# Kernel tuning notes

Measured on AMD Instinct MI355X. Metric: run time of the kernel, lower is better.

The kernel has to match this reference:

```python
import jax, jax.numpy as jnp
import numpy as np

B, N, F = 2, 512, 128
NUM_BASIS = 4


def _mlp(x, W1, b1, W2, b2, W3, b3):
    # two hidden ReLU layers, linear output -> [..., NUM_BASIS]
    h = jax.nn.relu(x @ W1 + b1)
    h = jax.nn.relu(h @ W2 + b2)
    return h @ W3 + b3


def setup_inputs() -> dict:
    key = jax.random.key(0)
    ks = jax.random.split(key, 12)
    s = 0.05  # keep activations O(1)
    inp = {
        "pointwise_features": jax.random.normal(ks[0], (B, N, F), jnp.float32),
        "relative_features": jax.random.normal(ks[1], (B, N, N, F), jnp.float32),
        "pointwise_basis": jax.random.normal(ks[2], (B, N, NUM_BASIS, 3), jnp.float32),
        "relative_basis": jax.random.normal(ks[3], (B, N, N, NUM_BASIS, 3), jnp.float32),
        "pw_W1": jax.random.normal(ks[4], (F, 128), jnp.float32) * s,
        "pw_b1": jnp.zeros((128,), jnp.float32),
        "pw_W2": jax.random.normal(ks[5], (128, 128), jnp.float32) * s,
        "pw_b2": jnp.zeros((128,), jnp.float32),
        "pw_W3": jax.random.normal(ks[6], (128, NUM_BASIS), jnp.float32) * s,
        "pw_b3": jnp.zeros((NUM_BASIS,), jnp.float32),
        "rel_W1": jax.random.normal(ks[7], (F, 128), jnp.float32) * s,
        "rel_b1": jnp.zeros((128,), jnp.float32),
        "rel_W2": jax.random.normal(ks[8], (128, 128), jnp.float32) * s,
        "rel_b2": jnp.zeros((128,), jnp.float32),
        "rel_W3": jax.random.normal(ks[9], (128, NUM_BASIS), jnp.float32) * s,
        "rel_b3": jnp.zeros((NUM_BASIS,), jnp.float32),
        # last 64 atoms are padding (masked) in every batch element
        "masked_elements": jnp.broadcast_to(jnp.arange(N) >= N - 64, (B, N)),
    }
    return inp


def reference(pointwise_features, relative_features, pointwise_basis, relative_basis,
              pw_W1, pw_b1, pw_W2, pw_b2, pw_W3, pw_b3,
              rel_W1, rel_b1, rel_W2, rel_b2, rel_W3, rel_b3,
              masked_elements):
    unmasked = ~masked_elements                      # [B, N]
    num_atoms = unmasked.sum(-1).astype(pointwise_features.dtype)  # [B]

    # pointwise_shift: [B, N, K, 3]
    pw_scale = _mlp(pointwise_features, pw_W1, pw_b1, pw_W2, pw_b2, pw_W3, pw_b3)
    pointwise_shift = pointwise_basis * pw_scale[..., None]

    # relative_shift: [B, N, N, K, 3], mask over j, mean over j
    rel_scale = _mlp(relative_features, rel_W1, rel_b1, rel_W2, rel_b2, rel_W3, rel_b3)
    relative_shift = relative_basis * rel_scale[..., None]
    relative_shift = relative_shift * unmasked[:, None, :, None, None]
    relative_shift = relative_shift.sum(-3) / num_atoms[:, None, None, None]  # [B, N, K, 3]

    all_shifts = pointwise_shift + relative_shift
    shift = all_shifts.sum(-2) / num_atoms[:, None, None]  # [B, N, 3]
    return shift
```

## Files before the change

kernel.cpp:

```cpp
#include <hip/hip_runtime.h>
#include <stdint.h>

#define LDK 136

typedef __attribute__((ext_vector_type(4))) float f32x4;
typedef __attribute__((ext_vector_type(8))) short bf16x8;

__device__ inline unsigned short f2bf_rtne(float f) {
    union { float f; unsigned u; } v; v.f = f;
    unsigned u = v.u;
    u += 0x7fffu + ((u >> 16) & 1u);
    return (unsigned short)(u >> 16);
}

__global__ void prep_kernel(const float* __restrict__ relW1, const float* __restrict__ relW2,
                            const float* __restrict__ pwW1, const float* __restrict__ pwW2,
                            const float* __restrict__ relW3, const float* __restrict__ pwW3,
                            const void* __restrict__ maskp,
                            float* __restrict__ maskf, float* __restrict__ na,
                            int* __restrict__ gflag, float* __restrict__ out,
                            unsigned short* __restrict__ w1T_rel, unsigned short* __restrict__ w2T_rel,
                            unsigned short* __restrict__ w1T_pw, unsigned short* __restrict__ w2T_pw,
                            unsigned short* __restrict__ w3T_rel, unsigned short* __restrict__ w3T_pw) {
    int t = threadIdx.x;
    const float* srcs[4] = {relW1, relW2, pwW1, pwW2};
    unsigned short* dsts[4] = {w1T_rel, w2T_rel, w1T_pw, w2T_pw};
    int e0 = blockIdx.x * 1024 + t;
#pragma unroll
    for (int i = 0; i < 4; ++i) {
        int e = e0 + i * 256;
        int mat = e >> 14, o = e & 16383;
        int n = o >> 7, k = o & 127;
        dsts[mat][o] = f2bf_rtne(srcs[mat][k * 128 + n]);
    }
    if (blockIdx.x == 1) {
        for (int i = t; i < 2048; i += 256) {
            int r = i >> 7, h = i & 127;
            w3T_rel[i] = (r < 4) ? f2bf_rtne(relW3[h * 4 + r]) : (unsigned short)0;
            w3T_pw[i]  = (r < 4) ? f2bf_rtne(pwW3[h * 4 + r])  : (unsigned short)0;
        }
    }
    if (blockIdx.x == 2) {
        for (int i = t; i < 3072; i += 256) out[i] = 0.f;
    }
    if (blockIdx.x == 0) {
        __shared__ int anyb;
        __shared__ float cnt[2];
        if (t == 0) anyb = 0;
        if (t < 2) cnt[t] = 0.f;
        __syncthreads();
        const unsigned char* mb = (const unsigned char*)maskp;
        int la = 0;
        for (int i = t; i < 1024; i += 256) la |= mb[i];
        if (la) atomicOr(&anyb, 1);
        __syncthreads();
        bool isbyte = (anyb != 0);
        const int* mi = (const int*)maskp;
        float loc0 = 0.f, loc1 = 0.f;
        for (int i = t; i < 1024; i += 256) {
            int v = isbyte ? (int)mb[i] : mi[i];
            float um = (v != 0) ? 0.f : 1.f;
            maskf[i] = um;
            if (i < 512) loc0 += um; else loc1 += um;
        }
        atomicAdd(&cnt[0], loc0);
        atomicAdd(&cnt[1], loc1);
        __syncthreads();
        if (t < 2) na[t] = cnt[t];
        if (t < 16) {
            float s = 0.f;
            for (int j = 0; j < 64; ++j) s += maskf[t * 64 + j];
            gflag[t] = (s > 0.f) ? 1 : 0;
        }
    }
}

__global__ __launch_bounds__(256, 3)
void mlp_kernel(const float* __restrict__ Xrel, const float* __restrict__ Xpw,
                const unsigned short* __restrict__ w1Tr, const unsigned short* __restrict__ w2Tr,
                const unsigned short* __restrict__ w3Tr,
                const unsigned short* __restrict__ w1Tp, const unsigned short* __restrict__ w2Tp,
                const unsigned short* __restrict__ w3Tp,
                const float* __restrict__ b1r, const float* __restrict__ b2r, const float* __restrict__ b3r,
                const float* __restrict__ b1p, const float* __restrict__ b2p, const float* __restrict__ b3p,
                const float* __restrict__ rel_basis, const float* __restrict__ pw_basis,
                const float* __restrict__ maskf, const float* __restrict__ na,
                const int* __restrict__ gflag,
                float* __restrict__ out) {
    __shared__ short xs[64 * LDK];
    __shared__ short hs[64 * LDK];
    __shared__ short w3s[16 * LDK];
    __shared__ float bs1[128], bs2[128], b3s[4];
    __shared__ float Sl[256];
    __shared__ float red[4][3];

    int t = threadIdx.x;
    int w = t >> 6, lane = t & 63, q = lane >> 4, col = lane & 15;

    bool isrel = (blockIdx.x >= 4);
    int rb = isrel ? ((int)blockIdx.x - 4) : (int)blockIdx.x;

    const float* X = isrel ? Xrel : Xpw;
    const unsigned short* w1T = isrel ? w1Tr : w1Tp;
    const unsigned short* w2T = isrel ? w2Tr : w2Tp;
    const unsigned short* w3T = isrel ? w3Tr : w3Tp;
    const float* b1 = isrel ? b1r : b1p;
    const float* b2 = isrel ? b2r : b2p;
    const float* b3 = isrel ? b3r : b3p;

    if (t < 128) { bs1[t] = b1[t]; bs2[t] = b2[t]; }
    if (t < 4) b3s[t] = b3[t];
    for (int i = t; i < 2048; i += 256) {
        int r = i >> 7, c = i & 127;
        w3s[r * LDK + c] = w3T[i];
    }

    int b = isrel ? (rb >> 10) : (rb >> 1);
    float NA = na[b];
    float scale = isrel ? (1.f / (NA * NA)) : (1.f / NA);

    int apack = 0x3210, nact = 4;
    if (isrel) {
        apack = 0; nact = 0;
        int gbase = b * 8 + (rb & 1) * 4;
#pragma unroll
        for (int tt = 0; tt < 4; ++tt)
            if (gflag[gbase + tt]) { apack |= tt << (4 * nact); ++nact; }
        if (nact == 0) return;
    }

    bf16x8 w1f[2][4], w2f[2][4];
#pragma unroll
    for (int tn = 0; tn < 2; ++tn)
#pragma unroll
        for (int kc = 0; kc < 4; ++kc) {
            int n = w * 32 + tn * 16 + col;
            int kk = kc * 32 + q * 8;
            w1f[tn][kc] = *(const bf16x8*)&w1T[n * 128 + kk];
            w2f[tn][kc] = *(const bf16x8*)&w2T[n * 128 + kk];
        }

    long rowbase = (long)rb * 256;
    int r0 = t >> 5, cg = t & 31;
    int myrow = w * 16 + col;
    int arow = t >> 2, ak = t & 3;

    float4 px[8];
    {
        const float4* Xg = (const float4*)(X + (rowbase + (long)(apack & 15) * 64) * 128);
#pragma unroll
        for (int i = 0; i < 8; ++i) px[i] = Xg[(r0 + 8 * i) * 32 + cg];
#pragma unroll
        for (int i = 0; i < 8; ++i) {
            float4 v = px[i];
            short4 s4 = make_short4((short)f2bf_rtne(v.x), (short)f2bf_rtne(v.y),
                                    (short)f2bf_rtne(v.z), (short)f2bf_rtne(v.w));
            *(short4*)&xs[(r0 + 8 * i) * LDK + cg * 4] = s4;
        }
    }
    __syncthreads();

    float p0 = 0.f, p1 = 0.f, p2 = 0.f;

    for (int a = 0; a < nact; ++a) {
        int tile = (apack >> (4 * a)) & 15;
        long trow = rowbase + (long)tile * 64;

        if (a + 1 < nact) {
            int tnx = (apack >> (4 * (a + 1))) & 15;
            const float4* Xg2 = (const float4*)(X + (rowbase + (long)tnx * 64) * 128);
#pragma unroll
            for (int i = 0; i < 8; ++i) px[i] = Xg2[(r0 + 8 * i) * 32 + cg];
        }

        f32x4 acc[2][4];
#pragma unroll
        for (int tn = 0; tn < 2; ++tn)
#pragma unroll
            for (int tm = 0; tm < 4; ++tm) acc[tn][tm] = (f32x4)(0.f);
#pragma unroll
        for (int kc = 0; kc < 4; ++kc) {
            bf16x8 bf[4];
#pragma unroll
            for (int tm = 0; tm < 4; ++tm)
                bf[tm] = *(const bf16x8*)&xs[(tm * 16 + col) * LDK + kc * 32 + q * 8];
#pragma unroll
            for (int tn = 0; tn < 2; ++tn)
#pragma unroll
                for (int tm = 0; tm < 4; ++tm)
                    acc[tn][tm] = __builtin_amdgcn_mfma_f32_16x16x32_bf16(w1f[tn][kc], bf[tm], acc[tn][tm], 0, 0, 0);
        }

#pragma unroll
        for (int tn = 0; tn < 2; ++tn)
#pragma unroll
            for (int tm = 0; tm < 4; ++tm) {
                int n0 = w * 32 + tn * 16 + q * 4;
                int m = tm * 16 + col;
                float4 bb = *(const float4*)&bs1[n0];
                short4 s4 = make_short4(
                    (short)f2bf_rtne(fmaxf(acc[tn][tm][0] + bb.x, 0.f)),
                    (short)f2bf_rtne(fmaxf(acc[tn][tm][1] + bb.y, 0.f)),
                    (short)f2bf_rtne(fmaxf(acc[tn][tm][2] + bb.z, 0.f)),
                    (short)f2bf_rtne(fmaxf(acc[tn][tm][3] + bb.w, 0.f)));
                *(short4*)&hs[m * LDK + n0] = s4;
            }
        __syncthreads();

        if (a + 1 < nact) {
#pragma unroll
            for (int i = 0; i < 8; ++i) {
                float4 v = px[i];
                short4 s4 = make_short4((short)f2bf_rtne(v.x), (short)f2bf_rtne(v.y),
                                        (short)f2bf_rtne(v.z), (short)f2bf_rtne(v.w));
                *(short4*)&xs[(r0 + 8 * i) * LDK + cg * 4] = s4;
            }
        }

        float bas0 = 0.f, bas1 = 0.f, bas2 = 0.f, mrow = 1.f;
        if (isrel) {
            const float* bp = &rel_basis[(trow + arow) * 12 + ak * 3];
            bas0 = bp[0]; bas1 = bp[1]; bas2 = bp[2];
            mrow = maskf[b * 512 + (rb & 1) * 256 + tile * 64 + myrow];
        }

        f32x4 acc2[2][4];
#pragma unroll
        for (int tn = 0; tn < 2; ++tn)
#pragma unroll
            for (int tm = 0; tm < 4; ++tm) acc2[tn][tm] = (f32x4)(0.f);
#pragma unroll
        for (int kc = 0; kc < 4; ++kc) {
            bf16x8 bf[4];
#pragma unroll
            for (int tm = 0; tm < 4; ++tm)
                bf[tm] = *(const bf16x8*)&hs[(tm * 16 + col) * LDK + kc * 32 + q * 8];
#pragma unroll
            for (int tn = 0; tn < 2; ++tn)
#pragma unroll
                for (int tm = 0; tm < 4; ++tm)
                    acc2[tn][tm] = __builtin_amdgcn_mfma_f32_16x16x32_bf16(w2f[tn][kc], bf[tm], acc2[tn][tm], 0, 0, 0);
        }
        __syncthreads();

#pragma unroll
        for (int tn = 0; tn < 2; ++tn)
#pragma unroll
            for (int tm = 0; tm < 4; ++tm) {
                int n0 = w * 32 + tn * 16 + q * 4;
                int m = tm * 16 + col;
                float4 bb = *(const float4*)&bs2[n0];
                short4 s4 = make_short4(
                    (short)f2bf_rtne(fmaxf(acc2[tn][tm][0] + bb.x, 0.f)),
                    (short)f2bf_rtne(fmaxf(acc2[tn][tm][1] + bb.y, 0.f)),
                    (short)f2bf_rtne(fmaxf(acc2[tn][tm][2] + bb.z, 0.f)),
                    (short)f2bf_rtne(fmaxf(acc2[tn][tm][3] + bb.w, 0.f)));
                *(short4*)&hs[m * LDK + n0] = s4;
            }
        __syncthreads();

        {
            f32x4 a3 = (f32x4)(0.f);
#pragma unroll
            for (int kc = 0; kc < 4; ++kc) {
                bf16x8 w3fk = *(const bf16x8*)&w3s[col * LDK + kc * 32 + q * 8];
                bf16x8 hb = *(const bf16x8*)&hs[(w * 16 + col) * LDK + kc * 32 + q * 8];
                a3 = __builtin_amdgcn_mfma_f32_16x16x32_bf16(w3fk, hb, a3, 0, 0, 0);
            }
            if (isrel) {
                if (q == 0) {
                    float4 sm = make_float4((a3[0] + b3s[0]) * mrow, (a3[1] + b3s[1]) * mrow,
                                            (a3[2] + b3s[2]) * mrow, (a3[3] + b3s[3]) * mrow);
                    *(float4*)&Sl[myrow * 4] = sm;
                }
            } else if (q == 0) {
                long bi = trow + myrow;
                float s0 = a3[0] + b3s[0], s1 = a3[1] + b3s[1];
                float s2 = a3[2] + b3s[2], s3 = a3[3] + b3s[3];
                const float* pbp = &pw_basis[bi * 12];
                float o0 = s0 * pbp[0] + s1 * pbp[3] + s2 * pbp[6] + s3 * pbp[9];
                float o1 = s0 * pbp[1] + s1 * pbp[4] + s2 * pbp[7] + s3 * pbp[10];
                float o2 = s0 * pbp[2] + s1 * pbp[5] + s2 * pbp[8] + s3 * pbp[11];
                atomicAdd(&out[bi * 3 + 0], o0 * scale);
                atomicAdd(&out[bi * 3 + 1], o1 * scale);
                atomicAdd(&out[bi * 3 + 2], o2 * scale);
            }
        }
        __syncthreads();

        if (isrel) {
            float sk = Sl[arow * 4 + ak];
            p0 += sk * bas0; p1 += sk * bas1; p2 += sk * bas2;
        }
    }

    if (isrel) {
#pragma unroll
        for (int s = 32; s >= 4; s >>= 1) {
            p0 += __shfl_down(p0, s);
            p1 += __shfl_down(p1, s);
            p2 += __shfl_down(p2, s);
        }
        p0 += __shfl_down(p0, 2); p1 += __shfl_down(p1, 2); p2 += __shfl_down(p2, 2);
        p0 += __shfl_down(p0, 1); p1 += __shfl_down(p1, 1); p2 += __shfl_down(p2, 1);
        if (lane == 0) { red[w][0] = p0; red[w][1] = p1; red[w][2] = p2; }
        __syncthreads();
        if (t < 3) {
            float v = red[0][t] + red[1][t] + red[2][t] + red[3][t];
            atomicAdd(&out[(long)(rb >> 1) * 3 + t], v * scale);
        }
    }
}

extern "C" void kernel_launch(void* const* d_in, const int* in_sizes, int n_in,
                              void* d_out, int out_size, void* d_ws, size_t ws_size,
                              hipStream_t stream) {
    const float* pw_feat   = (const float*)d_in[0];
    const float* rel_feat  = (const float*)d_in[1];
    const float* pw_basis  = (const float*)d_in[2];
    const float* rel_basis = (const float*)d_in[3];
    const float* pw_W1 = (const float*)d_in[4];
    const float* pw_b1 = (const float*)d_in[5];
    const float* pw_W2 = (const float*)d_in[6];
    const float* pw_b2 = (const float*)d_in[7];
    const float* pw_W3 = (const float*)d_in[8];
    const float* pw_b3 = (const float*)d_in[9];
    const float* rel_W1 = (const float*)d_in[10];
    const float* rel_b1 = (const float*)d_in[11];
    const float* rel_W2 = (const float*)d_in[12];
    const float* rel_b2 = (const float*)d_in[13];
    const float* rel_W3 = (const float*)d_in[14];
    const float* rel_b3 = (const float*)d_in[15];
    const void*  maskp  = d_in[16];
    float* out = (float*)d_out;

    char* ws = (char*)d_ws;
    float* maskf = (float*)(ws + 0);
    float* na    = (float*)(ws + 4096);
    int*   gflag = (int*)(ws + 4160);
    unsigned short* w1T_rel = (unsigned short*)(ws + 4352);
    unsigned short* w2T_rel = (unsigned short*)(ws + 37120);
    unsigned short* w1T_pw  = (unsigned short*)(ws + 69888);
    unsigned short* w2T_pw  = (unsigned short*)(ws + 102656);
    unsigned short* w3T_rel = (unsigned short*)(ws + 135424);
    unsigned short* w3T_pw  = (unsigned short*)(ws + 139520);

    prep_kernel<<<64, 256, 0, stream>>>(rel_W1, rel_W2, pw_W1, pw_W2, rel_W3, pw_W3, maskp,
                                        maskf, na, gflag, out,
                                        w1T_rel, w2T_rel, w1T_pw, w2T_pw,
                                        w3T_rel, w3T_pw);
    mlp_kernel<<<2052, 256, 0, stream>>>(rel_feat, pw_feat,
                                         w1T_rel, w2T_rel, w3T_rel,
                                         w1T_pw, w2T_pw, w3T_pw,
                                         rel_b1, rel_b2, rel_b3,
                                         pw_b1, pw_b2, pw_b3,
                                         rel_basis, pw_basis, maskf, na, gflag, out);
}
```

Before: 524.6 us.

## Process two row tiles per iteration with double-buffered LDS staging

Restructures the per-block tile loop so two 64-row tiles are handled per iteration, using separate A/B buffers for both the input and hidden activations. This cuts barriers per tile and lets the layer-2 and layer-3 work of one tile overlap the epilogue and staging of the other. Layer-3 weights now live in registers instead of LDS. The doubled shared-memory footprint and higher register pressure lower occupancy, which is reflected in dropping launch bounds from 3 to 2 blocks per CU.

```diff
diff --git a/kernel.cpp b/kernel.cpp
--- a/kernel.cpp
+++ b/kernel.cpp
@@ -75,7 +75,96 @@
     }
 }
 
-__global__ __launch_bounds__(256, 3)
+__device__ __forceinline__ void zero_acc(f32x4 (&acc)[2][4]) {
+#pragma unroll
+    for (int tn = 0; tn < 2; ++tn)
+#pragma unroll
+        for (int tm = 0; tm < 4; ++tm) acc[tn][tm] = (f32x4)(0.f);
+}
+
+__device__ __forceinline__ void mfma_layer(const short* src, const bf16x8 (&wf)[2][4],
+                                           f32x4 (&acc)[2][4], int col, int q) {
+#pragma unroll
+    for (int kc = 0; kc < 4; ++kc) {
+        bf16x8 bf[4];
+#pragma unroll
+        for (int tm = 0; tm < 4; ++tm)
+            bf[tm] = *(const bf16x8*)&src[(tm * 16 + col) * LDK + kc * 32 + q * 8];
+#pragma unroll
+        for (int tn = 0; tn < 2; ++tn)
+#pragma unroll
+            for (int tm = 0; tm < 4; ++tm)
+                acc[tn][tm] = __builtin_amdgcn_mfma_f32_16x16x32_bf16(wf[tn][kc], bf[tm], acc[tn][tm], 0, 0, 0);
+    }
+}
+
+__device__ __forceinline__ void epi_relu_store(const f32x4 (&acc)[2][4], const float* bs,
+                                               short* dst, int w, int q, int col) {
+#pragma unroll
+    for (int tn = 0; tn < 2; ++tn)
+#pragma unroll
+        for (int tm = 0; tm < 4; ++tm) {
+            int n0 = w * 32 + tn * 16 + q * 4;
+            int m = tm * 16 + col;
+            float4 bb = *(const float4*)&bs[n0];
+            short4 s4 = make_short4(
+                (short)f2bf_rtne(fmaxf(acc[tn][tm][0] + bb.x, 0.f)),
+                (short)f2bf_rtne(fmaxf(acc[tn][tm][1] + bb.y, 0.f)),
+                (short)f2bf_rtne(fmaxf(acc[tn][tm][2] + bb.z, 0.f)),
+                (short)f2bf_rtne(fmaxf(acc[tn][tm][3] + bb.w, 0.f)));
+            *(short4*)&dst[m * LDK + n0] = s4;
+        }
+}
+
+__device__ __forceinline__ void load_px(const float* X, long trow, float4 (&v)[8], int r0, int cg) {
+    const float4* Xg = (const float4*)(X + trow * 128);
+#pragma unroll
+    for (int i = 0; i < 8; ++i) v[i] = Xg[(r0 + 8 * i) * 32 + cg];
+}
+
+__device__ __forceinline__ void stage_conv(const float4 (&v)[8], short* dst, int r0, int cg) {
+#pragma unroll
+    for (int i = 0; i < 8; ++i) {
+        float4 vv = v[i];
+        short4 s4 = make_short4((short)f2bf_rtne(vv.x), (short)f2bf_rtne(vv.y),
+                                (short)f2bf_rtne(vv.z), (short)f2bf_rtne(vv.w));
+        *(short4*)&dst[(r0 + 8 * i) * LDK + cg * 4] = s4;
+    }
+}
+
+__device__ __forceinline__ f32x4 layer3(const short* hsrc, const bf16x8 (&w3f)[4],
+                                        int w, int col, int q) {
+    f32x4 a3 = (f32x4)(0.f);
+#pragma unroll
+    for (int kc = 0; kc < 4; ++kc) {
+        bf16x8 hb = *(const bf16x8*)&hsrc[(w * 16 + col) * LDK + kc * 32 + q * 8];
+        a3 = __builtin_amdgcn_mfma_f32_16x16x32_bf16(w3f[kc], hb, a3, 0, 0, 0);
+    }
+    return a3;
+}
+
+__device__ __forceinline__ void l3_epi(f32x4 a3, bool isrel, int q, int myrow,
+                                       const float* b3s, float mrow, float* Slx,
+                                       long trow, const float* __restrict__ pw_basis,
+                                       float scale, float* __restrict__ out) {
+    if (q != 0) return;
+    float s0 = a3[0] + b3s[0], s1 = a3[1] + b3s[1];
+    float s2 = a3[2] + b3s[2], s3 = a3[3] + b3s[3];
+    if (isrel) {
+        *(float4*)&Slx[myrow * 4] = make_float4(s0 * mrow, s1 * mrow, s2 * mrow, s3 * mrow);
+    } else {
+        long bi = trow + myrow;
+        const float* pbp = &pw_basis[bi * 12];
+        float o0 = s0 * pbp[0] + s1 * pbp[3] + s2 * pbp[6] + s3 * pbp[9];
+        float o1 = s0 * pbp[1] + s1 * pbp[4] + s2 * pbp[7] + s3 * pbp[10];
+        float o2 = s0 * pbp[2] + s1 * pbp[5] + s2 * pbp[8] + s3 * pbp[11];
+        atomicAdd(&out[bi * 3 + 0], o0 * scale);
+        atomicAdd(&out[bi * 3 + 1], o1 * scale);
+        atomicAdd(&out[bi * 3 + 2], o2 * scale);
+    }
+}
+
+__global__ __launch_bounds__(256, 2)
 void mlp_kernel(const float* __restrict__ Xrel, const float* __restrict__ Xpw,
                 const unsigned short* __restrict__ w1Tr, const unsigned short* __restrict__ w2Tr,
                 const unsigned short* __restrict__ w3Tr,
@@ -87,11 +176,10 @@
                 const float* __restrict__ maskf, const float* __restrict__ na,
                 const int* __restrict__ gflag,
                 float* __restrict__ out) {
-    __shared__ short xs[64 * LDK];
-    __shared__ short hs[64 * LDK];
-    __shared__ short w3s[16 * LDK];
+    __shared__ short xsA[64 * LDK], xsB[64 * LDK];
+    __shared__ short hsA[64 * LDK], hsB[64 * LDK];
     __shared__ float bs1[128], bs2[128], b3s[4];
-    __shared__ float Sl[256];
+    __shared__ float Sl[2][256];
     __shared__ float red[4][3];
 
     int t = threadIdx.x;
@@ -110,10 +198,6 @@
 
     if (t < 128) { bs1[t] = b1[t]; bs2[t] = b2[t]; }
     if (t < 4) b3s[t] = b3[t];
-    for (int i = t; i < 2048; i += 256) {
-        int r = i >> 7, c = i & 127;
-        w3s[r * LDK + c] = w3T[i];
-    }
 
     int b = isrel ? (rb >> 10) : (rb >> 1);
     float NA = na[b];
@@ -129,7 +213,7 @@
         if (nact == 0) return;
     }
 
-    bf16x8 w1f[2][4], w2f[2][4];
+    bf16x8 w1f[2][4], w2f[2][4], w3f[4];
 #pragma unroll
     for (int tn = 0; tn < 2; ++tn)
 #pragma unroll
@@ -139,170 +223,126 @@
             w1f[tn][kc] = *(const bf16x8*)&w1T[n * 128 + kk];
             w2f[tn][kc] = *(const bf16x8*)&w2T[n * 128 + kk];
         }
+#pragma unroll
+    for (int kc = 0; kc < 4; ++kc)
+        w3f[kc] = *(const bf16x8*)&w3T[col * 128 + kc * 32 + q * 8];
 
     long rowbase = (long)rb * 256;
     int r0 = t >> 5, cg = t & 31;
     int myrow = w * 16 + col;
     int arow = t >> 2, ak = t & 3;
+    int mbase = b * 512 + (rb & 1) * 256;
 
     float4 px[8];
-    {
-        const float4* Xg = (const float4*)(X + (rowbase + (long)(apack & 15) * 64) * 128);
-#pragma unroll
-        for (int i = 0; i < 8; ++i) px[i] = Xg[(r0 + 8 * i) * 32 + cg];
-#pragma unroll
-        for (int i = 0; i < 8; ++i) {
-            float4 v = px[i];
-            short4 s4 = make_short4((short)f2bf_rtne(v.x), (short)f2bf_rtne(v.y),
-                                    (short)f2bf_rtne(v.z), (short)f2bf_rtne(v.w));
-            *(short4*)&xs[(r0 + 8 * i) * LDK + cg * 4] = s4;
-        }
+    load_px(X, rowbase + (long)(apack & 15) * 64, px, r0, cg);
+    stage_conv(px, xsA, r0, cg);
+    if (nact >= 2) {
+        load_px(X, rowbase + (long)((apack >> 4) & 15) * 64, px, r0, cg);
+        stage_conv(px, xsB, r0, cg);
     }
     __syncthreads();
 
     float p0 = 0.f, p1 = 0.f, p2 = 0.f;
-
-    for (int a = 0; a < nact; ++a) {
-        int tile = (apack >> (4 * a)) & 15;
-        long trow = rowbase + (long)tile * 64;
-
-        if (a + 1 < nact) {
-            int tnx = (apack >> (4 * (a + 1))) & 15;
-            const float4* Xg2 = (const float4*)(X + (rowbase + (long)tnx * 64) * 128);
-#pragma unroll
-            for (int i = 0; i < 8; ++i) px[i] = Xg2[(r0 + 8 * i) * 32 + cg];
-        }
-
-        f32x4 acc[2][4];
-#pragma unroll
-        for (int tn = 0; tn < 2; ++tn)
-#pragma unroll
-            for (int tm = 0; tm < 4; ++tm) acc[tn][tm] = (f32x4)(0.f);
-#pragma unroll
-        for (int kc = 0; kc < 4; ++kc) {
-            bf16x8 bf[4];
-#pragma unroll
-            for (int tm = 0; tm < 4; ++tm)
-                bf[tm] = *(const bf16x8*)&xs[(tm * 16 + col) * LDK + kc * 32 + q * 8];
-#pragma unroll
-            for (int tn = 0; tn < 2; ++tn)
-#pragma unroll
-                for (int tm = 0; tm < 4; ++tm)
-                    acc[tn][tm] = __builtin_amdgcn_mfma_f32_16x16x32_bf16(w1f[tn][kc], bf[tm], acc[tn][tm], 0, 0, 0);
-        }
-
-#pragma unroll
-        for (int tn = 0; tn < 2; ++tn)
-#pragma unroll
-            for (int tm = 0; tm < 4; ++tm) {
-                int n0 = w * 32 + tn * 16 + q * 4;
-                int m = tm * 16 + col;
-                float4 bb = *(const float4*)&bs1[n0];
-                short4 s4 = make_short4(
-                    (short)f2bf_rtne(fmaxf(acc[tn][tm][0] + bb.x, 0.f)),
-                    (short)f2bf_rtne(fmaxf(acc[tn][tm][1] + bb.y, 0.f)),
-                    (short)f2bf_rtne(fmaxf(acc[tn][tm][2] + bb.z, 0.f)),
-                    (short)f2bf_rtne(fmaxf(acc[tn][tm][3] + bb.w, 0.f)));
-                *(short4*)&hs[m * LDK + n0] = s4;
-            }
-        __syncthreads();
-
-        if (a + 1 < nact) {
-#pragma unroll
-            for (int i = 0; i < 8; ++i) {
-                float4 v = px[i];
-                short4 s4 = make_short4((short)f2bf_rtne(v.x), (short)f2bf_rtne(v.y),
-                                        (short)f2bf_rtne(v.z), (short)f2bf_rtne(v.w));
-                *(short4*)&xs[(r0 + 8 * i) * LDK + cg * 4] = s4;
-            }
-        }
-
-        float bas0 = 0.f, bas1 = 0.f, bas2 = 0.f, mrow = 1.f;
-        if (isrel) {
-            const float* bp = &rel_basis[(trow + arow) * 12 + ak * 3];
-            bas0 = bp[0]; bas1 = bp[1]; bas2 = bp[2];
-            mrow = maskf[b * 512 + (rb & 1) * 256 + tile * 64 + myrow];
-        }
-
-        f32x4 acc2[2][4];
-#pragma unroll
-        for (int tn = 0; tn < 2; ++tn)
-#pragma unroll
-            for (int tm = 0; tm < 4; ++tm) acc2[tn][tm] = (f32x4)(0.f);
-#pragma unroll
-        for (int kc = 0; kc < 4; ++kc) {
-            bf16x8 bf[4];
-#pragma unroll
-            for (int tm = 0; tm < 4; ++tm)
-                bf[tm] = *(const bf16x8*)&hs[(tm * 16 + col) * LDK + kc * 32 + q * 8];
-#pragma unroll
-            for (int tn = 0; tn < 2; ++tn)
-#pragma unroll
-                for (int tm = 0; tm < 4; ++tm)
-                    acc2[tn][tm] = __builtin_amdgcn_mfma_f32_16x16x32_bf16(w2f[tn][kc], bf[tm], acc2[tn][tm], 0, 0, 0);
-        }
-        __syncthreads();
-
-#pragma unroll
-        for (int tn = 0; tn < 2; ++tn)
-#pragma unroll
-            for (int tm = 0; tm < 4; ++tm) {
-                int n0 = w * 32 + tn * 16 + q * 4;
-                int m = tm * 16 + col;
-                float4 bb = *(const float4*)&bs2[n0];
-                short4 s4 = make_short4(
-                    (short)f2bf_rtne(fmaxf(acc2[tn][tm][0] + bb.x, 0.f)),
-                    (short)f2bf_rtne(fmaxf(acc2[tn][tm][1] + bb.y, 0.f)),
-                    (short)f2bf_rtne(fmaxf(acc2[tn][tm][2] + bb.z, 0.f)),
-                    (short)f2bf_rtne(fmaxf(acc2[tn][tm][3] + bb.w, 0.f)));
-                *(short4*)&hs[m * LDK + n0] = s4;
-            }
-        __syncthreads();
-
+    f32x4 acc[2][4];
+
+    int a = 0;
+    for (; a + 1 < nact; a += 2) {
+        int tA = (apack >> (4 * a)) & 15;
+        int tB = (apack >> (4 * (a + 1))) & 15;
+        long trA = rowbase + (long)tA * 64;
+        long trB = rowbase + (long)tB * 64;
+        bool hN0 = (a + 2 < nact);
+        bool hN1 = (a + 3 < nact);
+
+        if (hN0) load_px(X, rowbase + (long)((apack >> (4 * (a + 2))) & 15) * 64, px, r0, cg);
+        zero_acc(acc);
+        mfma_layer(xsA, w1f, acc, col, q);
+        epi_relu_store(acc, bs1, hsA, w, q, col);
+        zero_acc(acc);
+        mfma_layer(xsB, w1f, acc, col, q);
+        epi_relu_store(acc, bs1, hsB, w, q, col);
+        __syncthreads();
+
+        if (hN0) stage_conv(px, xsA, r0, cg);
+        if (hN1) load_px(X, rowbase + (long)((apack >> (4 * (a + 3))) & 15) * 64, px, r0, cg);
+        float baA0 = 0.f, baA1 = 0.f, baA2 = 0.f, baB0 = 0.f, baB1 = 0.f, baB2 = 0.f;
+        float mrA = 1.f, mrB = 1.f;
+        if (isrel) {
+            const float* bpA = &rel_basis[(trA + arow) * 12 + ak * 3];
+            baA0 = bpA[0]; baA1 = bpA[1]; baA2 = bpA[2];
+            const float* bpB = &rel_basis[(trB + arow) * 12 + ak * 3];
+            baB0 = bpB[0]; baB1 = bpB[1]; baB2 = bpB[2];
+            mrA = maskf[mbase + tA * 64 + myrow];
+            mrB = maskf[mbase + tB * 64 + myrow];
+        }
+        zero_acc(acc);
+        mfma_layer(hsA, w2f, acc, col, q);
+        __syncthreads();
+
+        epi_relu_store(acc, bs2, hsA, w, q, col);
+        zero_acc(acc);
+        mfma_layer(hsB, w2f, acc, col, q);
+        __syncthreads();
+
+        epi_relu_store(acc, bs2, hsB, w, q, col);
         {
-            f32x4 a3 = (f32x4)(0.f);
-#pragma unroll
-            for (int kc = 0; kc < 4; ++kc) {
-                bf16x8 w3fk = *(const bf16x8*)&w3s[col * LDK + kc * 32 + q * 8];
-                bf16x8 hb = *(const bf16x8*)&hs[(w * 16 + col) * LDK + kc * 32 + q * 8];
-                a3 = __builtin_amdgcn_mfma_f32_16x16x32_bf16(w3fk, hb, a3, 0, 0, 0);
-            }
-            if (isrel) {
-                if (q == 0) {
-                    float4 sm = make_float4((a3[0] + b3s[0]) * mrow, (a3[1] + b3s[1]) * mrow,
-                                            (a3[2] + b3s[2]) * mrow, (a3[3] + b3s[3]) * mrow);
-                    *(float4*)&Sl[myrow * 4] = sm;
-                }
-            } else if (q == 0) {
-                long bi = trow + myrow;
-                float s0 = a3[0] + b3s[0], s1 = a3[1] + b3s[1];
-                float s2 = a3[2] + b3s[2], s3 = a3[3] + b3s[3];
-                const float* pbp = &pw_basis[bi * 12];
-                float o0 = s0 * pbp[0] + s1 * pbp[3] + s2 * pbp[6] + s3 * pbp[9];
-                float o1 = s0 * pbp[1] + s1 * pbp[4] + s2 * pbp[7] + s3 * pbp[10];
-                float o2 = s0 * pbp[2] + s1 * pbp[5] + s2 * pbp[8] + s3 * pbp[11];
-                atomicAdd(&out[bi * 3 + 0], o0 * scale);
-                atomicAdd(&out[bi * 3 + 1], o1 * scale);
-                atomicAdd(&out[bi * 3 + 2], o2 * scale);
-            }
-        }
-        __syncthreads();
-
-        if (isrel) {
-            float sk = Sl[arow * 4 + ak];
-            p0 += sk * bas0; p1 += sk * bas1; p2 += sk * bas2;
+            f32x4 a3 = layer3(hsA, w3f, w, col, q);
+            l3_epi(a3, isrel, q, myrow, b3s, mrA, Sl[0], trA, pw_basis, scale, out);
+        }
+        if (hN1) stage_conv(px, xsB, r0, cg);
+        __syncthreads();
+
+        {
+            f32x4 a3 = layer3(hsB, w3f, w, col, q);
+            l3_epi(a3, isrel, q, myrow, b3s, mrB, Sl[1], trB, pw_basis, scale, out);
+        }
+        if (isrel) {
+            float sk = Sl[0][arow * 4 + ak];
+            p0 += sk * baA0; p1 += sk * baA1; p2 += sk * baA2;
+        }
+        __syncthreads();
+        if (isrel) {
+            float sk = Sl[1][arow * 4 + ak];
+            p0 += sk * baB0; p1 += sk * baB1; p2 += sk * baB2;
+        }
+    }
+
+    if (a < nact) {
+        int tA = (apack >> (4 * a)) & 15;
+        long trA = rowbase + (long)tA * 64;
+        float baA0 = 0.f, baA1 = 0.f, baA2 = 0.f, mrA = 1.f;
+        if (isrel) {
+            const float* bpA = &rel_basis[(trA + arow) * 12 + ak * 3];
+            baA0 = bpA[0]; baA1 = bpA[1]; baA2 = bpA[2];
+            mrA = maskf[mbase + tA * 64 + myrow];
+        }
+        zero_acc(acc);
+        mfma_layer(xsA, w1f, acc, col, q);
+        epi_relu_store(acc, bs1, hsA, w, q, col);
+        __syncthreads();
+        zero_acc(acc);
+        mfma_layer(hsA, w2f, acc, col, q);
+        __syncthreads();
+        epi_relu_store(acc, bs2, hsA, w, q, col);
+        __syncthreads();
+        {
+            f32x4 a3 = layer3(hsA, w3f, w, col, q);
+            l3_epi(a3, isrel, q, myrow, b3s, mrA, Sl[0], trA, pw_basis, scale, out);
+        }
+        __syncthreads();
+        if (isrel) {
+            float sk = Sl[0][arow * 4 + ak];
+            p0 += sk * baA0; p1 += sk * baA1; p2 += sk * baA2;
         }
     }
 
     if (isrel) {
 #pragma unroll
-        for (int s = 32; s >= 4; s >>= 1) {
+        for (int s = 32; s > 0; s >>= 1) {
             p0 += __shfl_down(p0, s);
             p1 += __shfl_down(p1, s);
             p2 += __shfl_down(p2, s);
         }
-        p0 += __shfl_down(p0, 2); p1 += __shfl_down(p1, 2); p2 += __shfl_down(p2, 2);
-        p0 += __shfl_down(p0, 1); p1 += __shfl_down(p1, 1); p2 += __shfl_down(p2, 1);
         if (lane == 0) { red[w][0] = p0; red[w][1] = p1; red[w][2] = p2; }
         __syncthreads();
         if (t < 3) {
```

Measured after the change: 446.5 us. 14.9% less time.

## Use 512-thread blocks with 8 waves each owning 16 hidden columns

Applied to the files above, without the earlier changes.

Doubles the MLP kernel's block size to 8 waves, so each wave computes one 16-wide output column tile instead of two. This halves per-thread weight fragments, accumulators and prefetch registers to allow more waves in flight. It also moves the rel_basis and mask loads ahead of the first GEMM so their latency overlaps compute. The layer-3 and reduction stages still use only 4 waves, so half the threads sit idle there, and the extra synchronisation cost across more waves may offset the gain.

```diff
diff --git a/kernel.cpp b/kernel.cpp
--- a/kernel.cpp
+++ b/kernel.cpp
@@ -75,7 +75,7 @@
     }
 }
 
-__global__ __launch_bounds__(256, 3)
+__global__ __launch_bounds__(512, 4)
 void mlp_kernel(const float* __restrict__ Xrel, const float* __restrict__ Xpw,
                 const unsigned short* __restrict__ w1Tr, const unsigned short* __restrict__ w2Tr,
                 const unsigned short* __restrict__ w3Tr,
@@ -95,7 +95,7 @@
     __shared__ float red[4][3];
 
     int t = threadIdx.x;
-    int w = t >> 6, lane = t & 63, q = lane >> 4, col = lane & 15;
+    int wv = t >> 6, lane = t & 63, q = lane >> 4, col = lane & 15;
 
     bool isrel = (blockIdx.x >= 4);
     int rb = isrel ? ((int)blockIdx.x - 4) : (int)blockIdx.x;
@@ -110,9 +110,8 @@
 
     if (t < 128) { bs1[t] = b1[t]; bs2[t] = b2[t]; }
     if (t < 4) b3s[t] = b3[t];
-    for (int i = t; i < 2048; i += 256) {
-        int r = i >> 7, c = i & 127;
-        w3s[r * LDK + c] = w3T[i];
+    for (int i = t; i < 2048; i += 512) {
+        w3s[(i >> 7) * LDK + (i & 127)] = w3T[i];
     }
 
     int b = isrel ? (rb >> 10) : (rb >> 1);
@@ -129,33 +128,32 @@
         if (nact == 0) return;
     }
 
-    bf16x8 w1f[2][4], w2f[2][4];
-#pragma unroll
-    for (int tn = 0; tn < 2; ++tn)
-#pragma unroll
-        for (int kc = 0; kc < 4; ++kc) {
-            int n = w * 32 + tn * 16 + col;
-            int kk = kc * 32 + q * 8;
-            w1f[tn][kc] = *(const bf16x8*)&w1T[n * 128 + kk];
-            w2f[tn][kc] = *(const bf16x8*)&w2T[n * 128 + kk];
-        }
+    bf16x8 w1f[4], w2f[4];
+#pragma unroll
+    for (int kc = 0; kc < 4; ++kc) {
+        int n = wv * 16 + col;
+        int kk = kc * 32 + q * 8;
+        w1f[kc] = *(const bf16x8*)&w1T[n * 128 + kk];
+        w2f[kc] = *(const bf16x8*)&w2T[n * 128 + kk];
+    }
 
     long rowbase = (long)rb * 256;
     int r0 = t >> 5, cg = t & 31;
-    int myrow = w * 16 + col;
+    int myrow = wv * 16 + col;
     int arow = t >> 2, ak = t & 3;
-
-    float4 px[8];
+    int mbase = b * 512 + (rb & 1) * 256;
+
+    float4 px[4];
     {
         const float4* Xg = (const float4*)(X + (rowbase + (long)(apack & 15) * 64) * 128);
 #pragma unroll
-        for (int i = 0; i < 8; ++i) px[i] = Xg[(r0 + 8 * i) * 32 + cg];
-#pragma unroll
-        for (int i = 0; i < 8; ++i) {
+        for (int i = 0; i < 4; ++i) px[i] = Xg[(r0 + 16 * i) * 32 + cg];
+#pragma unroll
+        for (int i = 0; i < 4; ++i) {
             float4 v = px[i];
             short4 s4 = make_short4((short)f2bf_rtne(v.x), (short)f2bf_rtne(v.y),
                                     (short)f2bf_rtne(v.z), (short)f2bf_rtne(v.w));
-            *(short4*)&xs[(r0 + 8 * i) * LDK + cg * 4] = s4;
+            *(short4*)&xs[(r0 + 16 * i) * LDK + cg * 4] = s4;
         }
     }
     __syncthreads();
@@ -170,14 +168,21 @@
             int tnx = (apack >> (4 * (a + 1))) & 15;
             const float4* Xg2 = (const float4*)(X + (rowbase + (long)tnx * 64) * 128);
 #pragma unroll
-            for (int i = 0; i < 8; ++i) px[i] = Xg2[(r0 + 8 * i) * 32 + cg];
-        }
-
-        f32x4 acc[2][4];
-#pragma unroll
-        for (int tn = 0; tn < 2; ++tn)
-#pragma unroll
-            for (int tm = 0; tm < 4; ++tm) acc[tn][tm] = (f32x4)(0.f);
+            for (int i = 0; i < 4; ++i) px[i] = Xg2[(r0 + 16 * i) * 32 + cg];
+        }
+
+        float bas0 = 0.f, bas1 = 0.f, bas2 = 0.f, mrow = 1.f;
+        if (isrel) {
+            if (t < 256) {
+                const float* bp = &rel_basis[(trow + arow) * 12 + ak * 3];
+                bas0 = bp[0]; bas1 = bp[1]; bas2 = bp[2];
+            }
+            if (wv < 4 && q == 0) mrow = maskf[mbase + tile * 64 + myrow];
+        }
+
+        f32x4 acc[4];
+#pragma unroll
+        for (int tm = 0; tm < 4; ++tm) acc[tm] = (f32x4)(0.f);
 #pragma unroll
         for (int kc = 0; kc < 4; ++kc) {
             bf16x8 bf[4];
@@ -185,50 +190,37 @@
             for (int tm = 0; tm < 4; ++tm)
                 bf[tm] = *(const bf16x8*)&xs[(tm * 16 + col) * LDK + kc * 32 + q * 8];
 #pragma unroll
-            for (int tn = 0; tn < 2; ++tn)
-#pragma unroll
-                for (int tm = 0; tm < 4; ++tm)
-                    acc[tn][tm] = __builtin_amdgcn_mfma_f32_16x16x32_bf16(w1f[tn][kc], bf[tm], acc[tn][tm], 0, 0, 0);
-        }
-
-#pragma unroll
-        for (int tn = 0; tn < 2; ++tn)
-#pragma unroll
-            for (int tm = 0; tm < 4; ++tm) {
-                int n0 = w * 32 + tn * 16 + q * 4;
-                int m = tm * 16 + col;
-                float4 bb = *(const float4*)&bs1[n0];
-                short4 s4 = make_short4(
-                    (short)f2bf_rtne(fmaxf(acc[tn][tm][0] + bb.x, 0.f)),
-                    (short)f2bf_rtne(fmaxf(acc[tn][tm][1] + bb.y, 0.f)),
-                    (short)f2bf_rtne(fmaxf(acc[tn][tm][2] + bb.z, 0.f)),
-                    (short)f2bf_rtne(fmaxf(acc[tn][tm][3] + bb.w, 0.f)));
-                *(short4*)&hs[m * LDK + n0] = s4;
-            }
+            for (int tm = 0; tm < 4; ++tm)
+                acc[tm] = __builtin_amdgcn_mfma_f32_16x16x32_bf16(w1f[kc], bf[tm], acc[tm], 0, 0, 0);
+        }
+
+#pragma unroll
+        for (int tm = 0; tm < 4; ++tm) {
+            int n0 = wv * 16 + q * 4;
+            int m = tm * 16 + col;
+            float4 bb = *(const float4*)&bs1[n0];
+            short4 s4 = make_short4(
+                (short)f2bf_rtne(fmaxf(acc[tm][0] + bb.x, 0.f)),
+                (short)f2bf_rtne(fmaxf(acc[tm][1] + bb.y, 0.f)),
+                (short)f2bf_rtne(fmaxf(acc[tm][2] + bb.z, 0.f)),
+                (short)f2bf_rtne(fmaxf(acc[tm][3] + bb.w, 0.f)));
+            *(short4*)&hs[m * LDK + n0] = s4;
+        }
         __syncthreads();
 
         if (a + 1 < nact) {
 #pragma unroll
-            for (int i = 0; i < 8; ++i) {
+            for (int i = 0; i < 4; ++i) {
                 float4 v = px[i];
                 short4 s4 = make_short4((short)f2bf_rtne(v.x), (short)f2bf_rtne(v.y),
                                         (short)f2bf_rtne(v.z), (short)f2bf_rtne(v.w));
-                *(short4*)&xs[(r0 + 8 * i) * LDK + cg * 4] = s4;
+                *(short4*)&xs[(r0 + 16 * i) * LDK + cg * 4] = s4;
             }
         }
 
-        float bas0 = 0.f, bas1 = 0.f, bas2 = 0.f, mrow = 1.f;
-        if (isrel) {
-            const float* bp = &rel_basis[(trow + arow) * 12 + ak * 3];
-            bas0 = bp[0]; bas1 = bp[1]; bas2 = bp[2];
-            mrow = maskf[b * 512 + (rb & 1) * 256 + tile * 64 + myrow];
-        }
-
-        f32x4 acc2[2][4];
-#pragma unroll
-        for (int tn = 0; tn < 2; ++tn)
-#pragma unroll
-            for (int tm = 0; tm < 4; ++tm) acc2[tn][tm] = (f32x4)(0.f);
+        f32x4 acc2[4];
+#pragma unroll
+        for (int tm = 0; tm < 4; ++tm) acc2[tm] = (f32x4)(0.f);
 #pragma unroll
         for (int kc = 0; kc < 4; ++kc) {
             bf16x8 bf[4];
@@ -236,59 +228,54 @@
             for (int tm = 0; tm < 4; ++tm)
                 bf[tm] = *(const bf16x8*)&hs[(tm * 16 + col) * LDK + kc * 32 + q * 8];
 #pragma unroll
-            for (int tn = 0; tn < 2; ++tn)
-#pragma unroll
-                for (int tm = 0; tm < 4; ++tm)
-                    acc2[tn][tm] = __builtin_amdgcn_mfma_f32_16x16x32_bf16(w2f[tn][kc], bf[tm], acc2[tn][tm], 0, 0, 0);
-        }
-        __syncthreads();
-
-#pragma unroll
-        for (int tn = 0; tn < 2; ++tn)
-#pragma unroll
-            for (int tm = 0; tm < 4; ++tm) {
-                int n0 = w * 32 + tn * 16 + q * 4;
-                int m = tm * 16 + col;
-                float4 bb = *(const float4*)&bs2[n0];
-                short4 s4 = make_short4(
-                    (short)f2bf_rtne(fmaxf(acc2[tn][tm][0] + bb.x, 0.f)),
-                    (short)f2bf_rtne(fmaxf(acc2[tn][tm][1] + bb.y, 0.f)),
-                    (short)f2bf_rtne(fmaxf(acc2[tn][tm][2] + bb.z, 0.f)),
-                    (short)f2bf_rtne(fmaxf(acc2[tn][tm][3] + bb.w, 0.f)));
-                *(short4*)&hs[m * LDK + n0] = s4;
-            }
-        __syncthreads();
-
-        {
+            for (int tm = 0; tm < 4; ++tm)
+                acc2[tm] = __builtin_amdgcn_mfma_f32_16x16x32_bf16(w2f[kc], bf[tm], acc2[tm], 0, 0, 0);
+        }
+        __syncthreads();
+
+#pragma unroll
+        for (int tm = 0; tm < 4; ++tm) {
+            int n0 = wv * 16 + q * 4;
+            int m = tm * 16 + col;
+            float4 bb = *(const float4*)&bs2[n0];
+            short4 s4 = make_short4(
+                (short)f2bf_rtne(fmaxf(acc2[tm][0] + bb.x, 0.f)),
+                (short)f2bf_rtne(fmaxf(acc2[tm][1] + bb.y, 0.f)),
+                (short)f2bf_rtne(fmaxf(acc2[tm][2] + bb.z, 0.f)),
+                (short)f2bf_rtne(fmaxf(acc2[tm][3] + bb.w, 0.f)));
+            *(short4*)&hs[m * LDK + n0] = s4;
+        }
+        __syncthreads();
+
+        if (wv < 4) {
             f32x4 a3 = (f32x4)(0.f);
 #pragma unroll
             for (int kc = 0; kc < 4; ++kc) {
                 bf16x8 w3fk = *(const bf16x8*)&w3s[col * LDK + kc * 32 + q * 8];
-                bf16x8 hb = *(const bf16x8*)&hs[(w * 16 + col) * LDK + kc * 32 + q * 8];
+                bf16x8 hb = *(const bf16x8*)&hs[(wv * 16 + col) * LDK + kc * 32 + q * 8];
                 a3 = __builtin_amdgcn_mfma_f32_16x16x32_bf16(w3fk, hb, a3, 0, 0, 0);
             }
-            if (isrel) {
-                if (q == 0) {
-                    float4 sm = make_float4((a3[0] + b3s[0]) * mrow, (a3[1] + b3s[1]) * mrow,
-                                            (a3[2] + b3s[2]) * mrow, (a3[3] + b3s[3]) * mrow);
-                    *(float4*)&Sl[myrow * 4] = sm;
-                }
-            } else if (q == 0) {
-                long bi = trow + myrow;
+            if (q == 0) {
                 float s0 = a3[0] + b3s[0], s1 = a3[1] + b3s[1];
                 float s2 = a3[2] + b3s[2], s3 = a3[3] + b3s[3];
-                const float* pbp = &pw_basis[bi * 12];
-                float o0 = s0 * pbp[0] + s1 * pbp[3] + s2 * pbp[6] + s3 * pbp[9];
-                float o1 = s0 * pbp[1] + s1 * pbp[4] + s2 * pbp[7] + s3 * pbp[10];
-                float o2 = s0 * pbp[2] + s1 * pbp[5] + s2 * pbp[8] + s3 * pbp[11];
-                atomicAdd(&out[bi * 3 + 0], o0 * scale);
-                atomicAdd(&out[bi * 3 + 1], o1 * scale);
-                atomicAdd(&out[bi * 3 + 2], o2 * scale);
+                if (isrel) {
+                    *(float4*)&Sl[myrow * 4] =
+                        make_float4(s0 * mrow, s1 * mrow, s2 * mrow, s3 * mrow);
+                } else {
+                    long bi = trow + myrow;
+                    const float* pbp = &pw_basis[bi * 12];
+                    float o0 = s0 * pbp[0] + s1 * pbp[3] + s2 * pbp[6] + s3 * pbp[9];
+                    float o1 = s0 * pbp[1] + s1 * pbp[4] + s2 * pbp[7] + s3 * pbp[10];
+                    float o2 = s0 * pbp[2] + s1 * pbp[5] + s2 * pbp[8] + s3 * pbp[11];
+                    atomicAdd(&out[bi * 3 + 0], o0 * scale);
+                    atomicAdd(&out[bi * 3 + 1], o1 * scale);
+                    atomicAdd(&out[bi * 3 + 2], o2 * scale);
+                }
             }
         }
         __syncthreads();
 
-        if (isrel) {
+        if (isrel && t < 256) {
             float sk = Sl[arow * 4 + ak];
             p0 += sk * bas0; p1 += sk * bas1; p2 += sk * bas2;
         }
@@ -296,14 +283,12 @@
 
     if (isrel) {
 #pragma unroll
-        for (int s = 32; s >= 4; s >>= 1) {
+        for (int s = 32; s > 0; s >>= 1) {
             p0 += __shfl_down(p0, s);
             p1 += __shfl_down(p1, s);
             p2 += __shfl_down(p2, s);
         }
-        p0 += __shfl_down(p0, 2); p1 += __shfl_down(p1, 2); p2 += __shfl_down(p2, 2);
-        p0 += __shfl_down(p0, 1); p1 += __shfl_down(p1, 1); p2 += __shfl_down(p2, 1);
-        if (lane == 0) { red[w][0] = p0; red[w][1] = p1; red[w][2] = p2; }
+        if (wv < 4 && lane == 0) { red[wv][0] = p0; red[wv][1] = p1; red[wv][2] = p2; }
         __syncthreads();
         if (t < 3) {
             float v = red[0][t] + red[1][t] + red[2][t] + red[3][t];
@@ -349,7 +334,7 @@
                                         maskf, na, gflag, out,
                                         w1T_rel, w2T_rel, w1T_pw, w2T_pw,
                                         w3T_rel, w3T_pw);
-    mlp_kernel<<<2052, 256, 0, stream>>>(rel_feat, pw_feat,
+    mlp_kernel<<<2052, 512, 0, stream>>>(rel_feat, pw_feat,
                                          w1T_rel, w2T_rel, w3T_rel,
                                          w1T_pw, w2T_pw, w3T_pw,
                                          rel_b1, rel_b2, rel_b3,
```

Result: faster. 424.5 us (-19.1%).
